# Performance work log

Hardware: AMD Instinct MI355X
Metric: run time of the kernel (lower is better)

The kernel has to match this reference:

```python
import jax, jax.numpy as jnp
import numpy as np

N = 100000      # nodes
E = 1250000     # edges
IN = 128        # in_channels
H = 64          # hidden_channels
L = 2           # num_layers (GCNConv count)
EPS = 1e-5      # BatchNorm eps


def setup_inputs() -> dict:
    key = jax.random.key(0)
    ks = jax.random.split(key, 10)
    x = jax.random.normal(ks[0], (N, IN), jnp.float32)
    edge_index = jax.random.randint(ks[1], (2, E), 0, N, dtype=jnp.int32)
    fc_w = jax.random.normal(ks[2], (IN, H), jnp.float32) / np.sqrt(IN)
    fc_b = jax.random.normal(ks[3], (H,), jnp.float32) * 0.01
    conv_w = jax.random.normal(ks[4], (L, H, H), jnp.float32) / np.sqrt(H)
    conv_b = jax.random.normal(ks[5], (L, H), jnp.float32) * 0.01
    bn_gamma = jnp.ones((L + 1, H), jnp.float32)
    bn_beta = jnp.zeros((L + 1, H), jnp.float32)
    bn_mean = jax.random.normal(ks[6], (L + 1, H), jnp.float32) * 0.1
    bn_var = jax.random.uniform(ks[7], (L + 1, H), jnp.float32) + 0.5
    return {"x": x, "edge_index": edge_index, "fc_w": fc_w, "fc_b": fc_b,
            "conv_w": conv_w, "conv_b": conv_b, "bn_gamma": bn_gamma,
            "bn_beta": bn_beta, "bn_mean": bn_mean, "bn_var": bn_var}


def reference(x, edge_index, fc_w, fc_b, conv_w, conv_b, bn_gamma, bn_beta, bn_mean, bn_var):
    n = x.shape[0]
    loops = jnp.arange(n, dtype=edge_index.dtype)
    src = jnp.concatenate([edge_index[0], loops])   # add self-loops (GCNConv default)
    dst = jnp.concatenate([edge_index[1], loops])
    # symmetric normalization: deg computed on destination, norm = d_s^-1/2 * d_d^-1/2
    deg = jax.ops.segment_sum(jnp.ones_like(dst, x.dtype), dst, num_segments=n)
    dis = jax.lax.rsqrt(deg)                        # deg >= 1 thanks to self-loops
    norm = dis[src] * dis[dst]                      # [E+N]

    def bn(h, i):  # eval-mode BatchNorm1d with running stats
        return (h - bn_mean[i]) * (bn_gamma[i] * jax.lax.rsqrt(bn_var[i] + EPS)) + bn_beta[i]

    h = jax.nn.relu(bn(x @ fc_w + fc_b, 0))         # [N, H]; dropout is identity in eval
    last = h
    for i in range(conv_w.shape[0]):
        hw = h @ conv_w[i]                          # GCNConv: transform then aggregate
        agg = jax.ops.segment_sum(hw[src] * norm[:, None], dst, num_segments=n) + conv_b[i]
        h = jax.nn.relu(bn(agg, i + 1)) + last      # residual to post-fc activation
    return h
```

## Files before the change

kernel.cpp:

```cpp
#include <hip/hip_runtime.h>

#define NNODES 100000
#define NEDGES 1250000
#define IN_CH 128
#define HID 64
#define BN_EPS 1e-5f

#define NPAD 100352
#define BIN_N 256
#define BINW 391
#define BIN_CHUNK 2048
#define BIN_BLOCKS 611
#define BIN_CAP_LDS 32
#define BIN_REGION 10000
#define GBLOCKS 3125
#define ELL_C 32
#define OVF_CAP 65536

typedef __attribute__((ext_vector_type(8))) short s16x8;
typedef __attribute__((ext_vector_type(4))) float f32x4;

__device__ __forceinline__ ushort f2bf(float f) {
    union { float f; unsigned int i; } c;
    c.f = f;
    unsigned int lsb = (c.i >> 16) & 1u;
    return (ushort)((c.i + 0x7FFFu + lsb) >> 16);
}
__device__ __forceinline__ float bf2f(ushort u) {
    union { unsigned int i; float f; } c;
    c.i = (unsigned int)u << 16;
    return c.f;
}
__device__ __forceinline__ float asf(unsigned int i) {
    union { unsigned int i; float f; } c;
    c.i = i;
    return c.f;
}

__device__ __forceinline__ void fill_direct(int d, int soff, int* cnt,
                                            int* ell, int* ovf_n, int2* ovf) {
    int slot = atomicAdd(&cnt[d], 1);
    if (slot < ELL_C) ell[(d << 5) + slot] = soff;
    else {
        int oi = atomicAdd(ovf_n, 1);
        if (oi < OVF_CAP) ovf[oi] = make_int2(d, soff);
    }
}

__global__ __launch_bounds__(256) void edge_bin(
        const int* __restrict__ src, const int* __restrict__ dst,
        unsigned int* __restrict__ staged, int* bin_n,
        int* cnt, int* __restrict__ ell, int* ovf_n, int2* __restrict__ ovf) {
    __shared__ unsigned int sbin[BIN_N][BIN_CAP_LDS];
    __shared__ int scnt[BIN_N];
    __shared__ int sbase[BIN_N];
    const int tid = threadIdx.x;
    scnt[tid] = 0;
    __syncthreads();

    const int base = blockIdx.x * (BIN_CHUNK / 4);
    const int4* dst4 = (const int4*)dst;
    const int4* src4 = (const int4*)src;
#pragma unroll
    for (int k = 0; k < BIN_CHUNK / 1024; ++k) {
        int i = base + k * 256 + tid;
        if (i < NEDGES / 4) {
            int4 dv = dst4[i];
            int4 sv = src4[i];
#define BIN_ONE(D, S)                                                       \
            {                                                               \
                int b_ = (D) / BINW;                                        \
                unsigned int pk_ = ((unsigned int)((D) - b_ * BINW) << 17)  \
                                   | (unsigned int)(S);                     \
                int sl_ = atomicAdd(&scnt[b_], 1);                          \
                if (sl_ < BIN_CAP_LDS) sbin[b_][sl_] = pk_;                 \
                else fill_direct((D), (S) << 7, cnt, ell, ovf_n, ovf);      \
            }
            BIN_ONE(dv.x, sv.x)
            BIN_ONE(dv.y, sv.y)
            BIN_ONE(dv.z, sv.z)
            BIN_ONE(dv.w, sv.w)
#undef BIN_ONE
        }
    }
    __syncthreads();
    {
        int c = scnt[tid];
        if (c > BIN_CAP_LDS) c = BIN_CAP_LDS;
        sbase[tid] = atomicAdd(&bin_n[tid], c);
    }
    __syncthreads();
    const int wave = tid >> 6;
    const int lane = tid & 63;
    for (int b = wave; b < BIN_N; b += 4) {
        int c = scnt[b];
        if (c > BIN_CAP_LDS) c = BIN_CAP_LDS;
        if (lane < c) {
            int g = sbase[b] + lane;
            unsigned int v = sbin[b][lane];
            if (g < BIN_REGION) {
                staged[(size_t)b * BIN_REGION + g] = v;
            } else {
                int d = b * BINW + (int)(v >> 17);
                fill_direct(d, (int)(v & 0x1FFFFu) << 7, cnt, ell, ovf_n, ovf);
            }
        }
    }
}

__global__ __launch_bounds__(256) void ell_fill(
        const unsigned int* __restrict__ staged, const int* __restrict__ bin_n,
        int* cnt, int* __restrict__ ell, int* ovf_n, int2* __restrict__ ovf) {
    const int b = blockIdx.x;
    int n = bin_n[b];
    if (n > BIN_REGION) n = BIN_REGION;
    const unsigned int* sp = staged + (size_t)b * BIN_REGION;
    const int lo = b * BINW;
    int i = threadIdx.x;
    for (; i + 768 < n; i += 1024) {
        unsigned int v0 = sp[i];
        unsigned int v1 = sp[i + 256];
        unsigned int v2 = sp[i + 512];
        unsigned int v3 = sp[i + 768];
        fill_direct(lo + (int)(v0 >> 17), (int)(v0 & 0x1FFFFu) << 7, cnt, ell, ovf_n, ovf);
        fill_direct(lo + (int)(v1 >> 17), (int)(v1 & 0x1FFFFu) << 7, cnt, ell, ovf_n, ovf);
        fill_direct(lo + (int)(v2 >> 17), (int)(v2 & 0x1FFFFu) << 7, cnt, ell, ovf_n, ovf);
        fill_direct(lo + (int)(v3 >> 17), (int)(v3 & 0x1FFFFu) << 7, cnt, ell, ovf_n, ovf);
    }
    for (; i < n; i += 256) {
        unsigned int v = sp[i];
        fill_direct(lo + (int)(v >> 17), (int)(v & 0x1FFFFu) << 7, cnt, ell, ovf_n, ovf);
    }
}

__global__ __launch_bounds__(256) void fc_bn_relu(
        const float* __restrict__ x, const float* __restrict__ w,
        const float* __restrict__ b,
        const float* __restrict__ g, const float* __restrict__ be,
        const float* __restrict__ mu, const float* __restrict__ var,
        const int* __restrict__ cnt, float* __restrict__ dis,
        ushort* __restrict__ h0) {
    const int wave = threadIdx.x >> 6;
    const int lane = threadIdx.x & 63;
    const int m = lane & 15;
    const int q = lane >> 4;
    const int node_base = (blockIdx.x * 4 + wave) * 16;

    if (m == 0) {
#pragma unroll
        for (int r = 0; r < 4; ++r) {
            int node = node_base + q * 4 + r;
            if (node < NNODES) dis[node] = rsqrtf((float)(cnt[node] + 1));
        }
    }

    s16x8 bfrag[4][4];
#pragma unroll
    for (int kc = 0; kc < 4; ++kc)
#pragma unroll
        for (int ct = 0; ct < 4; ++ct)
#pragma unroll
            for (int j = 0; j < 8; ++j)
                bfrag[kc][ct][j] = (short)f2bf(w[(kc * 32 + q * 8 + j) * HID + ct * 16 + m]);

    f32x4 acc[4] = {{0,0,0,0},{0,0,0,0},{0,0,0,0},{0,0,0,0}};

    int row = node_base + m;
    if (row >= NNODES) row = NNODES - 1;
    const float4* xp = (const float4*)(x + (size_t)row * IN_CH + q * 8);

#pragma unroll
    for (int kc = 0; kc < 4; ++kc) {
        float4 a0 = xp[kc * 8 + 0];
        float4 a1 = xp[kc * 8 + 1];
        s16x8 af;
        af[0] = (short)f2bf(a0.x); af[1] = (short)f2bf(a0.y);
        af[2] = (short)f2bf(a0.z); af[3] = (short)f2bf(a0.w);
        af[4] = (short)f2bf(a1.x); af[5] = (short)f2bf(a1.y);
        af[6] = (short)f2bf(a1.z); af[7] = (short)f2bf(a1.w);
#pragma unroll
        for (int ct = 0; ct < 4; ++ct)
            acc[ct] = __builtin_amdgcn_mfma_f32_16x16x32_bf16(af, bfrag[kc][ct], acc[ct], 0, 0, 0);
    }

#pragma unroll
    for (int ct = 0; ct < 4; ++ct) {
        int col = ct * 16 + m;
        float sc = g[col] * rsqrtf(var[col] + BN_EPS);
        float off = (b[col] - mu[col]) * sc + be[col];
#pragma unroll
        for (int r = 0; r < 4; ++r) {
            int node = node_base + q * 4 + r;
            if (node < NNODES)
                h0[(size_t)node * HID + col] =
                    f2bf(fmaxf(acc[ct][r] * sc + off, 0.f));
        }
    }
}

__global__ __launch_bounds__(256) void conv_mm(
        const ushort* __restrict__ h, const float* __restrict__ w,
        const float* __restrict__ dis, ushort* __restrict__ hws) {
    const int wave = threadIdx.x >> 6;
    const int lane = threadIdx.x & 63;
    const int m = lane & 15;
    const int q = lane >> 4;
    const int node_base = (blockIdx.x * 4 + wave) * 16;

    s16x8 bfrag[2][4];
#pragma unroll
    for (int kc = 0; kc < 2; ++kc)
#pragma unroll
        for (int ct = 0; ct < 4; ++ct)
#pragma unroll
            for (int j = 0; j < 8; ++j)
                bfrag[kc][ct][j] = (short)f2bf(w[(kc * 32 + q * 8 + j) * HID + ct * 16 + m]);

    f32x4 acc[4] = {{0,0,0,0},{0,0,0,0},{0,0,0,0},{0,0,0,0}};

    int row = node_base + m;
    if (row >= NNODES) row = NNODES - 1;

#pragma unroll
    for (int kc = 0; kc < 2; ++kc) {
        const s16x8* hp = (const s16x8*)(h + (size_t)row * HID + kc * 32 + q * 8);
        s16x8 af = *hp;
#pragma unroll
        for (int ct = 0; ct < 4; ++ct)
            acc[ct] = __builtin_amdgcn_mfma_f32_16x16x32_bf16(af, bfrag[kc][ct], acc[ct], 0, 0, 0);
    }

    float dv[4];
#pragma unroll
    for (int r = 0; r < 4; ++r) {
        int node = node_base + q * 4 + r;
        dv[r] = (node < NNODES) ? dis[node] : 0.f;
    }
#pragma unroll
    for (int ct = 0; ct < 4; ++ct) {
#pragma unroll
        for (int r = 0; r < 4; ++r) {
            int node = node_base + q * 4 + r;
            if (node < NNODES)
                hws[(size_t)node * HID + ct * 16 + m] = f2bf(acc[ct][r] * dv[r]);
        }
    }
}

__global__ __launch_bounds__(256) void gather_update(
        const ushort* __restrict__ hws,
        const int* __restrict__ cnt, const int* __restrict__ ell,
        const int* __restrict__ ovf_n, const int2* __restrict__ ovf,
        const float* __restrict__ dis,
        const float* __restrict__ bias,
        const float* __restrict__ g, const float* __restrict__ be,
        const float* __restrict__ mu, const float* __restrict__ var,
        const ushort* __restrict__ last,
        ushort* __restrict__ out_bf, float* __restrict__ out_f,
        int write_f32) {
    const int wave = threadIdx.x >> 6;
    const int lane = threadIdx.x & 63;
    const int grp  = lane >> 3;
    const int j    = lane & 7;
    const int d = blockIdx.x * 32 + wave * 8 + grp;
    const unsigned int moff = (unsigned int)j * 16u;
    const unsigned int doff = ((unsigned int)d << 7) + moff;

    const char* hb = (const char*)hws;

    float a[8];
    {
        uint4 sv = *(const uint4*)(hb + doff);
        a[0] = asf(sv.x << 16); a[1] = asf(sv.x & 0xffff0000u);
        a[2] = asf(sv.y << 16); a[3] = asf(sv.y & 0xffff0000u);
        a[4] = asf(sv.z << 16); a[5] = asf(sv.z & 0xffff0000u);
        a[6] = asf(sv.w << 16); a[7] = asf(sv.w & 0xffff0000u);
    }

#define ACC8(V)                                                         \
    a[0] += asf((V).x << 16); a[1] += asf((V).x & 0xffff0000u);         \
    a[2] += asf((V).y << 16); a[3] += asf((V).y & 0xffff0000u);         \
    a[4] += asf((V).z << 16); a[5] += asf((V).z & 0xffff0000u);         \
    a[6] += asf((V).w << 16); a[7] += asf((V).w & 0xffff0000u);

    const int n = cnt[d];
    const int nn = (n < ELL_C) ? n : ELL_C;
    const int* sp = ell + ((size_t)d << 5);

    int k = 0;
    for (; k + 8 <= nn; k += 8) {
        unsigned int o0 = (unsigned int)sp[k + 0] + moff;
        unsigned int o1 = (unsigned int)sp[k + 1] + moff;
        unsigned int o2 = (unsigned int)sp[k + 2] + moff;
        unsigned int o3 = (unsigned int)sp[k + 3] + moff;
        unsigned int o4 = (unsigned int)sp[k + 4] + moff;
        unsigned int o5 = (unsigned int)sp[k + 5] + moff;
        unsigned int o6 = (unsigned int)sp[k + 6] + moff;
        unsigned int o7 = (unsigned int)sp[k + 7] + moff;
        uint4 v0 = *(const uint4*)(hb + o0);
        uint4 v1 = *(const uint4*)(hb + o1);
        uint4 v2 = *(const uint4*)(hb + o2);
        uint4 v3 = *(const uint4*)(hb + o3);
        uint4 v4 = *(const uint4*)(hb + o4);
        uint4 v5 = *(const uint4*)(hb + o5);
        uint4 v6 = *(const uint4*)(hb + o6);
        uint4 v7 = *(const uint4*)(hb + o7);
        ACC8(v0) ACC8(v1) ACC8(v2) ACC8(v3)
        ACC8(v4) ACC8(v5) ACC8(v6) ACC8(v7)
    }
    for (; k + 4 <= nn; k += 4) {
        unsigned int o0 = (unsigned int)sp[k + 0] + moff;
        unsigned int o1 = (unsigned int)sp[k + 1] + moff;
        unsigned int o2 = (unsigned int)sp[k + 2] + moff;
        unsigned int o3 = (unsigned int)sp[k + 3] + moff;
        uint4 v0 = *(const uint4*)(hb + o0);
        uint4 v1 = *(const uint4*)(hb + o1);
        uint4 v2 = *(const uint4*)(hb + o2);
        uint4 v3 = *(const uint4*)(hb + o3);
        ACC8(v0) ACC8(v1) ACC8(v2) ACC8(v3)
    }
    for (; k < nn; ++k) {
        uint4 v = *(const uint4*)(hb + ((unsigned int)sp[k] + moff));
        ACC8(v)
    }
    if (n > ELL_C) {
        int on = *ovf_n;
        if (on > OVF_CAP) on = OVF_CAP;
        for (int jj = 0; jj < on; ++jj) {
            int2 e = ovf[jj];
            if (e.x == d) {
                uint4 v = *(const uint4*)(hb + ((unsigned int)e.y + moff));
                ACC8(v)
            }
        }
    }
#undef ACC8

    float dd = dis[d];
    float4 bi0 = ((const float4*)bias)[2 * j], bi1 = ((const float4*)bias)[2 * j + 1];
    float4 g0  = ((const float4*)g)[2 * j],    g1  = ((const float4*)g)[2 * j + 1];
    float4 be0 = ((const float4*)be)[2 * j],   be1 = ((const float4*)be)[2 * j + 1];
    float4 mu0 = ((const float4*)mu)[2 * j],   mu1 = ((const float4*)mu)[2 * j + 1];
    float4 va0 = ((const float4*)var)[2 * j],  va1 = ((const float4*)var)[2 * j + 1];
    uint4 lv = *(const uint4*)((const char*)last + doff);
    float l0 = asf(lv.x << 16), l1 = asf(lv.x & 0xffff0000u);
    float l2 = asf(lv.y << 16), l3 = asf(lv.y & 0xffff0000u);
    float l4 = asf(lv.z << 16), l5 = asf(lv.z & 0xffff0000u);
    float l6 = asf(lv.w << 16), l7 = asf(lv.w & 0xffff0000u);

#define EPI(A, BI, GV, BE, MU, VA, LO) \
    (fmaxf(((A) * dd + (BI) - (MU)) * ((GV) * rsqrtf((VA) + BN_EPS)) + (BE), 0.f) + (LO))
    float r0 = EPI(a[0], bi0.x, g0.x, be0.x, mu0.x, va0.x, l0);
    float r1 = EPI(a[1], bi0.y, g0.y, be0.y, mu0.y, va0.y, l1);
    float r2 = EPI(a[2], bi0.z, g0.z, be0.z, mu0.z, va0.z, l2);
    float r3 = EPI(a[3], bi0.w, g0.w, be0.w, mu0.w, va0.w, l3);
    float r4 = EPI(a[4], bi1.x, g1.x, be1.x, mu1.x, va1.x, l4);
    float r5 = EPI(a[5], bi1.y, g1.y, be1.y, mu1.y, va1.y, l5);
    float r6 = EPI(a[6], bi1.z, g1.z, be1.z, mu1.z, va1.z, l6);
    float r7 = EPI(a[7], bi1.w, g1.w, be1.w, mu1.w, va1.w, l7);
#undef EPI

    if (write_f32) {
        float4* op = (float4*)(out_f + (size_t)d * HID + j * 8);
        op[0] = make_float4(r0, r1, r2, r3);
        op[1] = make_float4(r4, r5, r6, r7);
    } else {
        uint4 o;
        o.x = (unsigned int)f2bf(r0) | ((unsigned int)f2bf(r1) << 16);
        o.y = (unsigned int)f2bf(r2) | ((unsigned int)f2bf(r3) << 16);
        o.z = (unsigned int)f2bf(r4) | ((unsigned int)f2bf(r5) << 16);
        o.w = (unsigned int)f2bf(r6) | ((unsigned int)f2bf(r7) << 16);
        *(uint4*)((char*)out_bf + doff) = o;
    }
}

extern "C" void kernel_launch(void* const* d_in, const int* in_sizes, int n_in,
                              void* d_out, int out_size, void* d_ws, size_t ws_size,
                              hipStream_t stream) {
    const float* x      = (const float*)d_in[0];
    const int*   eidx   = (const int*)d_in[1];
    const float* fc_w   = (const float*)d_in[2];
    const float* fc_b   = (const float*)d_in[3];
    const float* conv_w = (const float*)d_in[4];
    const float* conv_b = (const float*)d_in[5];
    const float* bn_g   = (const float*)d_in[6];
    const float* bn_b   = (const float*)d_in[7];
    const float* bn_m   = (const float*)d_in[8];
    const float* bn_v   = (const float*)d_in[9];

    const int* src = eidx;
    const int* dst = eidx + NEDGES;

    float* out = (float*)d_out;

    float*  dis     = (float*)d_ws;
    int*    cnt     = (int*)(dis + NPAD);
    int*    meta    = cnt + NPAD;
    int*    ovf_n   = meta;
    int*    bin_n   = meta + 16;
    int2*   ovf     = (int2*)(meta + 272);
    int*    ell     = (int*)(ovf + OVF_CAP);
    ushort* h0      = (ushort*)(ell + (size_t)NNODES * ELL_C);
    ushort* h1      = h0 + (size_t)NNODES * HID;
    ushort* hws     = h1 + (size_t)NNODES * HID;
    unsigned int* staged = (unsigned int*)hws;

    const int BLK = 256;
    const int gridMM  = (NNODES + 63) / 64;

    hipMemsetAsync(cnt, 0, (size_t)NPAD * 4 + 272 * 4, stream);

    edge_bin<<<BIN_BLOCKS, BLK, 0, stream>>>(src, dst, staged, bin_n,
                                             cnt, ell, ovf_n, ovf);
    ell_fill<<<BIN_N, BLK, 0, stream>>>(staged, bin_n,
                                        cnt, ell, ovf_n, ovf);

    fc_bn_relu<<<gridMM, BLK, 0, stream>>>(x, fc_w, fc_b, bn_g, bn_b, bn_m, bn_v,
                                           cnt, dis, h0);

    conv_mm<<<gridMM, BLK, 0, stream>>>(h0, conv_w, dis, hws);
    gather_update<<<GBLOCKS, BLK, 0, stream>>>(hws, cnt, ell, ovf_n, ovf, dis,
                                               conv_b, bn_g + HID, bn_b + HID,
                                               bn_m + HID, bn_v + HID, h0,
                                               h1, nullptr, 0);

    conv_mm<<<gridMM, BLK, 0, stream>>>(h1, conv_w + HID * HID, dis, hws);
    gather_update<<<GBLOCKS, BLK, 0, stream>>>(hws, cnt, ell, ovf_n, ovf, dis,
                                               conv_b + HID, bn_g + 2 * HID, bn_b + 2 * HID,
                                               bn_m + 2 * HID, bn_v + 2 * HID, h0,
                                               nullptr, out, 1);
}
```

Before: 295.0 us.

## Fuse edge binning with FC and ELL fill with first conv matmul

Merges the edge-binning kernel with the FC+BN+ReLU kernel, and the ELL fill kernel with the first conv matmul, through block-index dispatch, so independent work shares a launch and overlaps. Degree counting moves to a separate atomic counter incremented during binning, so the degree is final before the ELL fill. The dis array is dropped and rsqrt(deg) is recomputed where needed. Staged data moves out of the hws buffer to avoid aliasing. It adds an extra global atomic per edge in the binning pass and an extra memset region.

```diff
diff --git a/kernel.cpp b/kernel.cpp
--- a/kernel.cpp
+++ b/kernel.cpp
@@ -13,6 +13,7 @@
 #define BIN_BLOCKS 611
 #define BIN_CAP_LDS 32
 #define BIN_REGION 10000
+#define MM_BLOCKS 1563
 #define GBLOCKS 3125
 #define ELL_C 32
 #define OVF_CAP 65536
@@ -37,24 +38,93 @@
     return c.f;
 }
 
-__device__ __forceinline__ void fill_direct(int d, int soff, int* cnt,
-                                            int* ell, int* ovf_n, int2* ovf) {
-    int slot = atomicAdd(&cnt[d], 1);
-    if (slot < ELL_C) ell[(d << 5) + slot] = soff;
+__device__ __forceinline__ void ell_insert(int d, int soff, int* slot,
+                                           int* ell, int* ovf_n, int2* ovf) {
+    int s = atomicAdd(&slot[d], 1);
+    if (s < ELL_C) ell[(d << 5) + s] = soff;
     else {
         int oi = atomicAdd(ovf_n, 1);
         if (oi < OVF_CAP) ovf[oi] = make_int2(d, soff);
     }
 }
 
-__global__ __launch_bounds__(256) void edge_bin(
+__device__ __forceinline__ void fc_body(
+        int blk, int tid,
+        const float* __restrict__ x, const float* __restrict__ w,
+        const float* __restrict__ b,
+        const float* __restrict__ g, const float* __restrict__ be,
+        const float* __restrict__ mu, const float* __restrict__ var,
+        ushort* __restrict__ h0) {
+    const int wave = tid >> 6;
+    const int lane = tid & 63;
+    const int m = lane & 15;
+    const int q = lane >> 4;
+    const int node_base = (blk * 4 + wave) * 16;
+
+    s16x8 bfrag[4][4];
+#pragma unroll
+    for (int kc = 0; kc < 4; ++kc)
+#pragma unroll
+        for (int ct = 0; ct < 4; ++ct)
+#pragma unroll
+            for (int j = 0; j < 8; ++j)
+                bfrag[kc][ct][j] = (short)f2bf(w[(kc * 32 + q * 8 + j) * HID + ct * 16 + m]);
+
+    f32x4 acc[4] = {{0,0,0,0},{0,0,0,0},{0,0,0,0},{0,0,0,0}};
+
+    int row = node_base + m;
+    if (row >= NNODES) row = NNODES - 1;
+    const float4* xp = (const float4*)(x + (size_t)row * IN_CH + q * 8);
+
+#pragma unroll
+    for (int kc = 0; kc < 4; ++kc) {
+        float4 a0 = xp[kc * 8 + 0];
+        float4 a1 = xp[kc * 8 + 1];
+        s16x8 af;
+        af[0] = (short)f2bf(a0.x); af[1] = (short)f2bf(a0.y);
+        af[2] = (short)f2bf(a0.z); af[3] = (short)f2bf(a0.w);
+        af[4] = (short)f2bf(a1.x); af[5] = (short)f2bf(a1.y);
+        af[6] = (short)f2bf(a1.z); af[7] = (short)f2bf(a1.w);
+#pragma unroll
+        for (int ct = 0; ct < 4; ++ct)
+            acc[ct] = __builtin_amdgcn_mfma_f32_16x16x32_bf16(af, bfrag[kc][ct], acc[ct], 0, 0, 0);
+    }
+
+#pragma unroll
+    for (int ct = 0; ct < 4; ++ct) {
+        int col = ct * 16 + m;
+        float sc = g[col] * rsqrtf(var[col] + BN_EPS);
+        float off = (b[col] - mu[col]) * sc + be[col];
+#pragma unroll
+        for (int r = 0; r < 4; ++r) {
+            int node = node_base + q * 4 + r;
+            if (node < NNODES)
+                h0[(size_t)node * HID + col] =
+                    f2bf(fmaxf(acc[ct][r] * sc + off, 0.f));
+        }
+    }
+}
+
+__global__ __launch_bounds__(256) void build_fc(
         const int* __restrict__ src, const int* __restrict__ dst,
         unsigned int* __restrict__ staged, int* bin_n,
-        int* cnt, int* __restrict__ ell, int* ovf_n, int2* __restrict__ ovf) {
+        int* cnt, int* slot, int* __restrict__ ell,
+        int* ovf_n, int2* __restrict__ ovf,
+        const float* __restrict__ x, const float* __restrict__ w,
+        const float* __restrict__ b,
+        const float* __restrict__ g, const float* __restrict__ be,
+        const float* __restrict__ mu, const float* __restrict__ var,
+        ushort* __restrict__ h0) {
     __shared__ unsigned int sbin[BIN_N][BIN_CAP_LDS];
     __shared__ int scnt[BIN_N];
     __shared__ int sbase[BIN_N];
     const int tid = threadIdx.x;
+
+    if (blockIdx.x >= BIN_BLOCKS) {
+        fc_body(blockIdx.x - BIN_BLOCKS, tid, x, w, b, g, be, mu, var, h0);
+        return;
+    }
+
     scnt[tid] = 0;
     __syncthreads();
 
@@ -69,12 +139,13 @@
             int4 sv = src4[i];
 #define BIN_ONE(D, S)                                                       \
             {                                                               \
+                atomicAdd(&cnt[(D)], 1);               \
                 int b_ = (D) / BINW;                                        \
                 unsigned int pk_ = ((unsigned int)((D) - b_ * BINW) << 17)  \
                                    | (unsigned int)(S);                     \
                 int sl_ = atomicAdd(&scnt[b_], 1);                          \
                 if (sl_ < BIN_CAP_LDS) sbin[b_][sl_] = pk_;                 \
-                else fill_direct((D), (S) << 7, cnt, ell, ovf_n, ovf);      \
+                else ell_insert((D), (S) << 7, slot, ell, ovf_n, ovf);      \
             }
             BIN_ONE(dv.x, sv.x)
             BIN_ONE(dv.y, sv.y)
@@ -92,25 +163,81 @@
     __syncthreads();
     const int wave = tid >> 6;
     const int lane = tid & 63;
-    for (int b = wave; b < BIN_N; b += 4) {
-        int c = scnt[b];
+    for (int bb = wave; bb < BIN_N; bb += 4) {
+        int c = scnt[bb];
         if (c > BIN_CAP_LDS) c = BIN_CAP_LDS;
         if (lane < c) {
-            int g = sbase[b] + lane;
-            unsigned int v = sbin[b][lane];
-            if (g < BIN_REGION) {
-                staged[(size_t)b * BIN_REGION + g] = v;
+            int gidx = sbase[bb] + lane;
+            unsigned int v = sbin[bb][lane];
+            if (gidx < BIN_REGION) {
+                staged[(size_t)bb * BIN_REGION + gidx] = v;
             } else {
-                int d = b * BINW + (int)(v >> 17);
-                fill_direct(d, (int)(v & 0x1FFFFu) << 7, cnt, ell, ovf_n, ovf);
+                int d = bb * BINW + (int)(v >> 17);
+                ell_insert(d, (int)(v & 0x1FFFFu) << 7, slot, ell, ovf_n, ovf);
             }
         }
     }
 }
 
-__global__ __launch_bounds__(256) void ell_fill(
+__device__ __forceinline__ void conv_body(
+        int blk, int tid,
+        const ushort* __restrict__ h, const float* __restrict__ w,
+        const int* __restrict__ cnt, ushort* __restrict__ hws) {
+    const int wave = tid >> 6;
+    const int lane = tid & 63;
+    const int m = lane & 15;
+    const int q = lane >> 4;
+    const int node_base = (blk * 4 + wave) * 16;
+
+    s16x8 bfrag[2][4];
+#pragma unroll
+    for (int kc = 0; kc < 2; ++kc)
+#pragma unroll
+        for (int ct = 0; ct < 4; ++ct)
+#pragma unroll
+            for (int j = 0; j < 8; ++j)
+                bfrag[kc][ct][j] = (short)f2bf(w[(kc * 32 + q * 8 + j) * HID + ct * 16 + m]);
+
+    f32x4 acc[4] = {{0,0,0,0},{0,0,0,0},{0,0,0,0},{0,0,0,0}};
+
+    int row = node_base + m;
+    if (row >= NNODES) row = NNODES - 1;
+
+#pragma unroll
+    for (int kc = 0; kc < 2; ++kc) {
+        const s16x8* hp = (const s16x8*)(h + (size_t)row * HID + kc * 32 + q * 8);
+        s16x8 af = *hp;
+#pragma unroll
+        for (int ct = 0; ct < 4; ++ct)
+            acc[ct] = __builtin_amdgcn_mfma_f32_16x16x32_bf16(af, bfrag[kc][ct], acc[ct], 0, 0, 0);
+    }
+
+    float dv[4];
+#pragma unroll
+    for (int r = 0; r < 4; ++r) {
+        int node = node_base + q * 4 + r;
+        dv[r] = (node < NNODES) ? rsqrtf((float)(cnt[node] + 1)) : 0.f;
+    }
+#pragma unroll
+    for (int ct = 0; ct < 4; ++ct) {
+#pragma unroll
+        for (int r = 0; r < 4; ++r) {
+            int node = node_base + q * 4 + r;
+            if (node < NNODES)
+                hws[(size_t)node * HID + ct * 16 + m] = f2bf(acc[ct][r] * dv[r]);
+        }
+    }
+}
+
+__global__ __launch_bounds__(256) void fill_conv(
         const unsigned int* __restrict__ staged, const int* __restrict__ bin_n,
-        int* cnt, int* __restrict__ ell, int* ovf_n, int2* __restrict__ ovf) {
+        int* slot, int* __restrict__ ell, int* ovf_n, int2* __restrict__ ovf,
+        const ushort* __restrict__ h, const float* __restrict__ w,
+        const int* __restrict__ cnt, ushort* __restrict__ hws) {
+    if (blockIdx.x >= BIN_N) {
+        conv_body(blockIdx.x - BIN_N, threadIdx.x, h, w, cnt, hws);
+        return;
+    }
     const int b = blockIdx.x;
     int n = bin_n[b];
     if (n > BIN_REGION) n = BIN_REGION;
@@ -122,128 +249,14 @@
         unsigned int v1 = sp[i + 256];
         unsigned int v2 = sp[i + 512];
         unsigned int v3 = sp[i + 768];
-        fill_direct(lo + (int)(v0 >> 17), (int)(v0 & 0x1FFFFu) << 7, cnt, ell, ovf_n, ovf);
-        fill_direct(lo + (int)(v1 >> 17), (int)(v1 & 0x1FFFFu) << 7, cnt, ell, ovf_n, ovf);
-        fill_direct(lo + (int)(v2 >> 17), (int)(v2 & 0x1FFFFu) << 7, cnt, ell, ovf_n, ovf);
-        fill_direct(lo + (int)(v3 >> 17), (int)(v3 & 0x1FFFFu) << 7, cnt, ell, ovf_n, ovf);
+        ell_insert(lo + (int)(v0 >> 17), (int)(v0 & 0x1FFFFu) << 7, slot, ell, ovf_n, ovf);
+        ell_insert(lo + (int)(v1 >> 17), (int)(v1 & 0x1FFFFu) << 7, slot, ell, ovf_n, ovf);
+        ell_insert(lo + (int)(v2 >> 17), (int)(v2 & 0x1FFFFu) << 7, slot, ell, ovf_n, ovf);
+        ell_insert(lo + (int)(v3 >> 17), (int)(v3 & 0x1FFFFu) << 7, slot, ell, ovf_n, ovf);
     }
     for (; i < n; i += 256) {
         unsigned int v = sp[i];
-        fill_direct(lo + (int)(v >> 17), (int)(v & 0x1FFFFu) << 7, cnt, ell, ovf_n, ovf);
-    }
-}
-
-__global__ __launch_bounds__(256) void fc_bn_relu(
-        const float* __restrict__ x, const float* __restrict__ w,
-        const float* __restrict__ b,
-        const float* __restrict__ g, const float* __restrict__ be,
-        const float* __restrict__ mu, const float* __restrict__ var,
-        const int* __restrict__ cnt, float* __restrict__ dis,
-        ushort* __restrict__ h0) {
-    const int wave = threadIdx.x >> 6;
-    const int lane = threadIdx.x & 63;
-    const int m = lane & 15;
-    const int q = lane >> 4;
-    const int node_base = (blockIdx.x * 4 + wave) * 16;
-
-    if (m == 0) {
-#pragma unroll
-        for (int r = 0; r < 4; ++r) {
-            int node = node_base + q * 4 + r;
-            if (node < NNODES) dis[node] = rsqrtf((float)(cnt[node] + 1));
-        }
-    }
-
-    s16x8 bfrag[4][4];
-#pragma unroll
-    for (int kc = 0; kc < 4; ++kc)
-#pragma unroll
-        for (int ct = 0; ct < 4; ++ct)
-#pragma unroll
-            for (int j = 0; j < 8; ++j)
-                bfrag[kc][ct][j] = (short)f2bf(w[(kc * 32 + q * 8 + j) * HID + ct * 16 + m]);
-
-    f32x4 acc[4] = {{0,0,0,0},{0,0,0,0},{0,0,0,0},{0,0,0,0}};
-
-    int row = node_base + m;
-    if (row >= NNODES) row = NNODES - 1;
-    const float4* xp = (const float4*)(x + (size_t)row * IN_CH + q * 8);
-
-#pragma unroll
-    for (int kc = 0; kc < 4; ++kc) {
-        float4 a0 = xp[kc * 8 + 0];
-        float4 a1 = xp[kc * 8 + 1];
-        s16x8 af;
-        af[0] = (short)f2bf(a0.x); af[1] = (short)f2bf(a0.y);
-        af[2] = (short)f2bf(a0.z); af[3] = (short)f2bf(a0.w);
-        af[4] = (short)f2bf(a1.x); af[5] = (short)f2bf(a1.y);
-        af[6] = (short)f2bf(a1.z); af[7] = (short)f2bf(a1.w);
-#pragma unroll
-        for (int ct = 0; ct < 4; ++ct)
-            acc[ct] = __builtin_amdgcn_mfma_f32_16x16x32_bf16(af, bfrag[kc][ct], acc[ct], 0, 0, 0);
-    }
-
-#pragma unroll
-    for (int ct = 0; ct < 4; ++ct) {
-        int col = ct * 16 + m;
-        float sc = g[col] * rsqrtf(var[col] + BN_EPS);
-        float off = (b[col] - mu[col]) * sc + be[col];
-#pragma unroll
-        for (int r = 0; r < 4; ++r) {
-            int node = node_base + q * 4 + r;
-            if (node < NNODES)
-                h0[(size_t)node * HID + col] =
-                    f2bf(fmaxf(acc[ct][r] * sc + off, 0.f));
-        }
-    }
-}
-
-__global__ __launch_bounds__(256) void conv_mm(
-        const ushort* __restrict__ h, const float* __restrict__ w,
-        const float* __restrict__ dis, ushort* __restrict__ hws) {
-    const int wave = threadIdx.x >> 6;
-    const int lane = threadIdx.x & 63;
-    const int m = lane & 15;
-    const int q = lane >> 4;
-    const int node_base = (blockIdx.x * 4 + wave) * 16;
-
-    s16x8 bfrag[2][4];
-#pragma unroll
-    for (int kc = 0; kc < 2; ++kc)
-#pragma unroll
-        for (int ct = 0; ct < 4; ++ct)
-#pragma unroll
-            for (int j = 0; j < 8; ++j)
-                bfrag[kc][ct][j] = (short)f2bf(w[(kc * 32 + q * 8 + j) * HID + ct * 16 + m]);
-
-    f32x4 acc[4] = {{0,0,0,0},{0,0,0,0},{0,0,0,0},{0,0,0,0}};
-
-    int row = node_base + m;
-    if (row >= NNODES) row = NNODES - 1;
-
-#pragma unroll
-    for (int kc = 0; kc < 2; ++kc) {
-        const s16x8* hp = (const s16x8*)(h + (size_t)row * HID + kc * 32 + q * 8);
-        s16x8 af = *hp;
-#pragma unroll
-        for (int ct = 0; ct < 4; ++ct)
-            acc[ct] = __builtin_amdgcn_mfma_f32_16x16x32_bf16(af, bfrag[kc][ct], acc[ct], 0, 0, 0);
-    }
-
-    float dv[4];
-#pragma unroll
-    for (int r = 0; r < 4; ++r) {
-        int node = node_base + q * 4 + r;
-        dv[r] = (node < NNODES) ? dis[node] : 0.f;
-    }
-#pragma unroll
-    for (int ct = 0; ct < 4; ++ct) {
-#pragma unroll
-        for (int r = 0; r < 4; ++r) {
-            int node = node_base + q * 4 + r;
-            if (node < NNODES)
-                hws[(size_t)node * HID + ct * 16 + m] = f2bf(acc[ct][r] * dv[r]);
-        }
+        ell_insert(lo + (int)(v >> 17), (int)(v & 0x1FFFFu) << 7, slot, ell, ovf_n, ovf);
     }
 }
 
@@ -251,7 +264,6 @@
         const ushort* __restrict__ hws,
         const int* __restrict__ cnt, const int* __restrict__ ell,
         const int* __restrict__ ovf_n, const int2* __restrict__ ovf,
-        const float* __restrict__ dis,
         const float* __restrict__ bias,
         const float* __restrict__ g, const float* __restrict__ be,
         const float* __restrict__ mu, const float* __restrict__ var,
@@ -336,7 +348,7 @@
     }
 #undef ACC8
 
-    float dd = dis[d];
+    float dd = rsqrtf((float)(n + 1));
     float4 bi0 = ((const float4*)bias)[2 * j], bi1 = ((const float4*)bias)[2 * j + 1];
     float4 g0  = ((const float4*)g)[2 * j],    g1  = ((const float4*)g)[2 * j + 1];
     float4 be0 = ((const float4*)be)[2 * j],   be1 = ((const float4*)be)[2 * j + 1];
@@ -372,6 +384,12 @@
         o.w = (unsigned int)f2bf(r6) | ((unsigned int)f2bf(r7) << 16);
         *(uint4*)((char*)out_bf + doff) = o;
     }
+}
+
+__global__ __launch_bounds__(256) void conv_mm(
+        const ushort* __restrict__ h, const float* __restrict__ w,
+        const int* __restrict__ cnt, ushort* __restrict__ hws) {
+    conv_body(blockIdx.x, threadIdx.x, h, w, cnt, hws);
 }
 
 extern "C" void kernel_launch(void* const* d_in, const int* in_sizes, int n_in,
@@ -393,9 +411,9 @@
 
     float* out = (float*)d_out;
 
-    float*  dis     = (float*)d_ws;
-    int*    cnt     = (int*)(dis + NPAD);
-    int*    meta    = cnt + NPAD;
+    int*    cnt     = (int*)d_ws;
+    int*    slot    = cnt + NPAD;
+    int*    meta    = slot + NPAD;
     int*    ovf_n   = meta;
     int*    bin_n   = meta + 16;
     int2*   ovf     = (int2*)(meta + 272);
@@ -403,29 +421,27 @@
     ushort* h0      = (ushort*)(ell + (size_t)NNODES * ELL_C);
     ushort* h1      = h0 + (size_t)NNODES * HID;
     ushort* hws     = h1 + (size_t)NNODES * HID;
-    unsigned int* staged = (unsigned int*)hws;
+    unsigned int* staged = (unsigned int*)(hws + (size_t)NNODES * HID);
 
     const int BLK = 256;
-    const int gridMM  = (NNODES + 63) / 64;
-
-    hipMemsetAsync(cnt, 0, (size_t)NPAD * 4 + 272 * 4, stream);
-
-    edge_bin<<<BIN_BLOCKS, BLK, 0, stream>>>(src, dst, staged, bin_n,
-                                             cnt, ell, ovf_n, ovf);
-    ell_fill<<<BIN_N, BLK, 0, stream>>>(staged, bin_n,
-                                        cnt, ell, ovf_n, ovf);
-
-    fc_bn_relu<<<gridMM, BLK, 0, stream>>>(x, fc_w, fc_b, bn_g, bn_b, bn_m, bn_v,
-                                           cnt, dis, h0);
-
-    conv_mm<<<gridMM, BLK, 0, stream>>>(h0, conv_w, dis, hws);
-    gather_update<<<GBLOCKS, BLK, 0, stream>>>(hws, cnt, ell, ovf_n, ovf, dis,
+
+    hipMemsetAsync(cnt, 0, (size_t)(2 * NPAD + 272) * 4, stream);
+
+    build_fc<<<BIN_BLOCKS + MM_BLOCKS, BLK, 0, stream>>>(
+        src, dst, staged, bin_n, cnt, slot, ell, ovf_n, ovf,
+        x, fc_w, fc_b, bn_g, bn_b, bn_m, bn_v, h0);
+
+    fill_conv<<<BIN_N + MM_BLOCKS, BLK, 0, stream>>>(
+        staged, bin_n, slot, ell, ovf_n, ovf, h0, conv_w, cnt, hws);
+
+    gather_update<<<GBLOCKS, BLK, 0, stream>>>(hws, cnt, ell, ovf_n, ovf,
                                                conv_b, bn_g + HID, bn_b + HID,
                                                bn_m + HID, bn_v + HID, h0,
                                                h1, nullptr, 0);
 
-    conv_mm<<<gridMM, BLK, 0, stream>>>(h1, conv_w + HID * HID, dis, hws);
-    gather_update<<<GBLOCKS, BLK, 0, stream>>>(hws, cnt, ell, ovf_n, ovf, dis,
+    conv_mm<<<MM_BLOCKS, BLK, 0, stream>>>(h1, conv_w + HID * HID, cnt, hws);
+
+    gather_update<<<GBLOCKS, BLK, 0, stream>>>(hws, cnt, ell, ovf_n, ovf,
                                                conv_b + HID, bn_g + 2 * HID, bn_b + 2 * HID,
                                                bn_m + 2 * HID, bn_v + 2 * HID, h0,
                                                nullptr, out, 1);
```

After: 317.2 us. 1.08x slower.
